# Optimization experiments

Measured on AMD Instinct MI355X. Metric: run time of the kernel, lower is better.

The kernel has to match this reference:

```python
import jax, jax.numpy as jnp
import numpy as np

EPS = 1e-5

def _conv(x, w, b, pad):
    y = jax.lax.conv_general_dilated(x, w, window_strides=(1, 1),
                                     padding=[(pad, pad), (pad, pad)],
                                     dimension_numbers=('NCHW', 'OIHW', 'NCHW'))
    return y + b[None, :, None, None]

def _bn_train(x, gamma, beta):
    # BatchNorm2d in training mode: batch statistics over (N,H,W), biased var
    mean = jnp.mean(x, axis=(0, 2, 3), keepdims=True)
    var = jnp.mean(jnp.square(x - mean), axis=(0, 2, 3), keepdims=True)
    xhat = (x - mean) * jax.lax.rsqrt(var + EPS)
    return xhat * gamma[None, :, None, None] + beta[None, :, None, None]

def _maxpool2(x):
    # CustomMaxPool2d(kernel=2) -> stride=2, no padding applied to data
    return jax.lax.reduce_window(x, -jnp.inf, jax.lax.max,
                                 (1, 1, 2, 2), (1, 1, 2, 2), 'VALID')

def setup_inputs() -> dict:
    key = jax.random.key(0)
    ks = jax.random.split(key, 12)
    B = 64
    d = jax.random.normal(ks[0], (B, 3, 224, 224), dtype=jnp.float32)
    def w_init(k, shape, fan_in):
        bound = 1.0 / np.sqrt(fan_in)
        return jax.random.uniform(k, shape, jnp.float32, -bound, bound)
    conv1_w = w_init(ks[1], (16, 3, 2, 2), 3 * 2 * 2)
    conv1_b = w_init(ks[2], (16,), 3 * 2 * 2)
    conv2_w = w_init(ks[3], (32, 16, 3, 3), 16 * 9)
    conv2_b = w_init(ks[4], (32,), 16 * 9)
    conv3_w = w_init(ks[5], (64, 32, 3, 3), 32 * 9)
    conv3_b = w_init(ks[6], (64,), 32 * 9)
    fc1_w = w_init(ks[7], (256, 64 * 28 * 28), 64 * 28 * 28)
    fc1_b = w_init(ks[8], (256,), 64 * 28 * 28)
    fc2_w = w_init(ks[9], (5, 256), 256)
    fc2_b = w_init(ks[10], (5,), 256)
    return dict(d=d,
                conv1_w=conv1_w, conv1_b=conv1_b,
                bn1_g=jnp.ones((16,), jnp.float32), bn1_b=jnp.zeros((16,), jnp.float32),
                conv2_w=conv2_w, conv2_b=conv2_b,
                bn2_g=jnp.ones((32,), jnp.float32), bn2_b=jnp.zeros((32,), jnp.float32),
                conv3_w=conv3_w, conv3_b=conv3_b,
                bn3_g=jnp.ones((64,), jnp.float32), bn3_b=jnp.zeros((64,), jnp.float32),
                fc1_w=fc1_w, fc1_b=fc1_b, fc2_w=fc2_w, fc2_b=fc2_b)

def reference(d, conv1_w, conv1_b, bn1_g, bn1_b,
              conv2_w, conv2_b, bn2_g, bn2_b,
              conv3_w, conv3_b, bn3_g, bn3_b,
              fc1_w, fc1_b, fc2_w, fc2_b):
    x = _maxpool2(jax.nn.relu(_bn_train(_conv(d, conv1_w, conv1_b, 1), bn1_g, bn1_b)))   # [B,16,112,112]
    x = _maxpool2(jax.nn.relu(_bn_train(_conv(x, conv2_w, conv2_b, 1), bn2_g, bn2_b)))   # [B,32,56,56]
    x = _maxpool2(jax.nn.relu(_bn_train(_conv(x, conv3_w, conv3_b, 1), bn3_g, bn3_b)))   # [B,64,28,28]
    x = x.reshape(x.shape[0], -1)                                                        # [B,50176]
    x = jax.nn.relu(x @ fc1_w.T + fc1_b)
    return x @ fc2_w.T + fc2_b                                                           # [B,5]
```

## Files before the change

### kernel.cpp

```cpp
#include <hip/hip_runtime.h>
#include <cstdint>
#include <cstddef>


typedef __attribute__((ext_vector_type(8))) short sh8_t;
typedef __attribute__((ext_vector_type(4))) float f4_t;
typedef unsigned short u16;
typedef unsigned int u32;

#define WS_X1   ((size_t)0)
#define WS_MX1  ((size_t)6422528)
#define WS_MN1  ((size_t)12845056)
#define WS_X2   ((size_t)19267584)
#define WS_MX2  ((size_t)22478848)
#define WS_MN2  ((size_t)25690112)
#define WS_X3T  ((size_t)28901376)
#define WS_MX3  ((size_t)30507008)
#define WS_MN3  ((size_t)32112640)
#define WS_WT1  ((size_t)33718272)
#define WS_WT2  ((size_t)33718784)
#define WS_WT3  ((size_t)33721856)
#define WS_P1   ((size_t)33731072)
#define WS_P2   ((size_t)35574272)
#define WS_P3   ((size_t)36377088)
#define WS_PD   ((size_t)36835840)
#define WS_ST   ((size_t)36839936)
#define WS_FCP  ((size_t)36840160)
#define WS_H1   ((size_t)37757664)

static __device__ __forceinline__ float4 ldg4(const float* p) {
  return *reinterpret_cast<const float4*>(p);
}
static __device__ __forceinline__ float bf2f(u16 u) {
  union { u32 i; float f; } c; c.i = ((u32)u) << 16; return c.f;
}
static __device__ __forceinline__ u16 f2bf(float f) {
  union { float f; u32 i; } c; c.f = f;
  const u32 x = c.i;
  return (u16)((x + 0x7fffu + ((x >> 16) & 1u)) >> 16);
}

__global__ __launch_bounds__(256)
void k_prep_w(const float* __restrict__ w1, const float* __restrict__ w2,
              const float* __restrict__ w3, u16* __restrict__ wt1,
              u16* __restrict__ wt2, u16* __restrict__ wt3) {
  const int t = blockIdx.x * 256 + threadIdx.x;
  if (t < 1024) {
    const int half = t >> 9;
    const int u = t & 511;
    const int co = u >> 5, k = u & 31;
    const int g = k >> 3, j = k & 7;
    const int kh = g >> 1, kw = g & 1;
    const int ci = (j < 4) ? j : j - 4;
    bool active = (j != 3) && (j != 7);
    if (half == 1) active = active && (j < 4);
    float val = 0.f;
    if (active) {
      const float w = w1[((co * 3 + ci) * 2 + kh) * 2 + kw];
      const u16 h = f2bf(w);
      val = (half == 0) ? bf2f(h) : (w - bf2f(h));
    }
    wt1[t] = f2bf(val);
  } else if (t < 7168) {
    const int u = t - 1024;
    const int ci = u & 15, kwp = (u >> 4) & 3, kh = (u >> 6) % 3, co = u / 192;
    float v = 0.f;
    if (kwp < 3) v = w2[((co * 16 + ci) * 3 + kh) * 3 + kwp];
    wt2[u] = f2bf(v);
  } else {
    const int u = t - 7168;
    const int ci = u & 31, kw = (u >> 5) % 3, kh = (u / 96) % 3, co = u / 288;
    wt3[u] = f2bf(w3[((co * 32 + ci) * 3 + kh) * 3 + kw]);
  }
}

__global__ __launch_bounds__(256)
void k_conv1(const float* __restrict__ d, const u16* __restrict__ wt1,
             const float* __restrict__ b1, u16* __restrict__ mx1,
             u16* __restrict__ mn1, float* __restrict__ part) {
  const int bx = blockIdx.x, by = blockIdx.y, n = blockIdx.z;
  const int ow0 = bx * 16, oh0 = by * 16;
  const int t = threadIdx.x, lane = t & 63, wv = t >> 6;
  const int g = lane >> 4, li = lane & 15;
  __shared__ __align__(16) u16 tile[18 * 18 * 8];
  for (int idx = t; idx < 324; idx += 256) {
    const int rr = idx / 18, cc = idx - rr * 18;
    const int ih = oh0 - 1 + rr, iw = ow0 - 1 + cc;
    float v[3] = {0.f, 0.f, 0.f};
    if ((unsigned)ih < 224u && (unsigned)iw < 224u) {
      #pragma unroll
      for (int ci = 0; ci < 3; ++ci)
        v[ci] = d[((size_t)(n * 3 + ci) * 224 + ih) * 224 + iw];
    }
    u16 rec[8];
    #pragma unroll
    for (int ci = 0; ci < 3; ++ci) {
      const u16 h = f2bf(v[ci]);
      rec[ci] = h;
      rec[4 + ci] = f2bf(v[ci] - bf2f(h));
    }
    rec[3] = 0; rec[7] = 0;
    u32 pk0 = (u32)rec[0] | ((u32)rec[1] << 16);
    u32 pk1 = (u32)rec[2] | ((u32)rec[3] << 16);
    u32 pk2 = (u32)rec[4] | ((u32)rec[5] << 16);
    u32 pk3 = (u32)rec[6] | ((u32)rec[7] << 16);
    *reinterpret_cast<int4*>(&tile[idx * 8]) = make_int4(pk0, pk1, pk2, pk3);
  }
  const sh8_t A1 = *reinterpret_cast<const sh8_t*>(wt1 + li * 32 + g * 8);
  const sh8_t A2 = *reinterpret_cast<const sh8_t*>(wt1 + 512 + li * 32 + g * 8);
  __syncthreads();
  const int kh = g >> 1, kw = g & 1;
  f4_t acc[4];
  #pragma unroll
  for (int r = 0; r < 4; ++r) acc[r] = (f4_t)0.f;
  #pragma unroll
  for (int r = 0; r < 4; ++r) {
    const int rr = wv * 4 + r + kh;
    const sh8_t B = *reinterpret_cast<const sh8_t*>(&tile[(rr * 18 + li + kw) * 8]);
    acc[r] = __builtin_amdgcn_mfma_f32_16x16x32_bf16(A1, B, acc[r], 0, 0, 0);
    acc[r] = __builtin_amdgcn_mfma_f32_16x16x32_bf16(A2, B, acc[r], 0, 0, 0);
  }
  const f4_t bias = *reinterpret_cast<const f4_t*>(b1 + 4 * g);
  f4_t y[4];
  #pragma unroll
  for (int r = 0; r < 4; ++r) y[r] = acc[r] + bias;
  const int ow = ow0 + li;
  {
    f4_t ssum = (f4_t)0.f, ssq = (f4_t)0.f;
    #pragma unroll
    for (int r = 0; r < 4; ++r) {
      const int oh = oh0 + wv * 4 + r;
      if (oh <= 224 && ow <= 224) { ssum += y[r]; ssq += y[r] * y[r]; }
    }
    #pragma unroll
    for (int m = 1; m < 16; m <<= 1)
      #pragma unroll
      for (int j = 0; j < 4; ++j) {
        ssum[j] += __shfl_xor(ssum[j], m);
        ssq[j]  += __shfl_xor(ssq[j], m);
      }
    if (li == 0) {
      const int slot = ((n * 15 + by) * 15 + bx) * 4 + wv;
      #pragma unroll
      for (int j = 0; j < 4; ++j) {
        part[(size_t)((4 * g + j) * 2 + 0) * 57600 + slot] = ssum[j];
        part[(size_t)((4 * g + j) * 2 + 1) * 57600 + slot] = ssq[j];
      }
    }
  }
  if (bx < 14 && by < 14) {
    #pragma unroll
    for (int rp = 0; rp < 2; ++rp) {
      f4_t vmax, vmin;
      #pragma unroll
      for (int j = 0; j < 4; ++j) {
        vmax[j] = fmaxf(y[2 * rp][j], y[2 * rp + 1][j]);
        vmin[j] = fminf(y[2 * rp][j], y[2 * rp + 1][j]);
      }
      f4_t omx, omn;
      #pragma unroll
      for (int j = 0; j < 4; ++j) {
        omx[j] = __shfl_xor(vmax[j], 1);
        omn[j] = __shfl_xor(vmin[j], 1);
      }
      if ((li & 1) == 0) {
        const int po = 8 * by + 2 * wv + rp, qo = 8 * bx + (li >> 1);
        const size_t off = ((size_t)((n * 112 + po) * 112 + qo)) * 16 + 4 * g;
        uint2 pmx, pmn;
        pmx.x = (u32)f2bf(fmaxf(vmax[0], omx[0])) | ((u32)f2bf(fmaxf(vmax[1], omx[1])) << 16);
        pmx.y = (u32)f2bf(fmaxf(vmax[2], omx[2])) | ((u32)f2bf(fmaxf(vmax[3], omx[3])) << 16);
        pmn.x = (u32)f2bf(fminf(vmin[0], omn[0])) | ((u32)f2bf(fminf(vmin[1], omn[1])) << 16);
        pmn.y = (u32)f2bf(fminf(vmin[2], omn[2])) | ((u32)f2bf(fminf(vmin[3], omn[3])) << 16);
        *reinterpret_cast<uint2*>(mx1 + off) = pmx;
        *reinterpret_cast<uint2*>(mn1 + off) = pmn;
      }
    }
  }
}

__global__ __launch_bounds__(256)
void k_fin1(const float* __restrict__ part, int P, int chunk, int S,
            double* __restrict__ p2) {
  const int c = blockIdx.x, s = blockIdx.y;
  const int start = s * chunk;
  const int end = min(P, start + chunk);
  __shared__ double rs[256], rq[256];
  double accs[2];
  #pragma unroll
  for (int mom = 0; mom < 2; ++mom) {
    const float* base = part + (size_t)(c * 2 + mom) * P;
    double a0 = 0.0, a1 = 0.0, a2 = 0.0, a3 = 0.0;
    int i = start + threadIdx.x * 4;
    for (; i + 3 < end; i += 1024) {
      const float4 v = ldg4(base + i);
      a0 += v.x; a1 += v.y; a2 += v.z; a3 += v.w;
    }
    for (int j = i; j < end && j < i + 4; ++j) a0 += base[j];
    accs[mom] = (a0 + a1) + (a2 + a3);
  }
  rs[threadIdx.x] = accs[0]; rq[threadIdx.x] = accs[1];
  __syncthreads();
  for (int off = 128; off > 0; off >>= 1) {
    if (threadIdx.x < off) {
      rs[threadIdx.x] += rs[threadIdx.x + off];
      rq[threadIdx.x] += rq[threadIdx.x + off];
    }
    __syncthreads();
  }
  if (threadIdx.x == 0) {
    p2[(size_t)(c * 2 + 0) * S + s] = rs[0];
    p2[(size_t)(c * 2 + 1) * S + s] = rq[0];
  }
}

__global__ __launch_bounds__(64)
void k_fin2(const double* __restrict__ p2, int S, double count,
            const float* __restrict__ g, const float* __restrict__ bta,
            float* __restrict__ scale, float* __restrict__ shift) {
  const int c = blockIdx.x, t = threadIdx.x;
  double s = 0.0, sq = 0.0;
  if (t < S) {
    s  = p2[(size_t)(c * 2 + 0) * S + t];
    sq = p2[(size_t)(c * 2 + 1) * S + t];
  }
  #pragma unroll
  for (int m = 1; m < 64; m <<= 1) {
    s  += __shfl_xor(s, m);
    sq += __shfl_xor(sq, m);
  }
  if (t == 0) {
    const double mean = s / count;
    const double var  = sq / count - mean * mean;
    const double rstd = 1.0 / sqrt(var + 1e-5);
    const double sc = (double)g[c] * rstd;
    scale[c] = (float)sc;
    shift[c] = (float)((double)bta[c] - mean * sc);
  }
}

template<int CH, int P>
__global__ __launch_bounds__(256)
void k_bnrelu(const u16* __restrict__ mx, const u16* __restrict__ mn,
              const float* __restrict__ scale, const float* __restrict__ shift,
              u16* __restrict__ xout) {
  constexpr int G = CH / 8;
  const int idx = blockIdx.x * 256 + threadIdx.x;
  const int cg = idx & (G - 1);
  int rest = idx / G;
  const int qo = rest % P; rest /= P;
  const int po = rest % P;
  const int n = rest / P;
  const size_t base = ((size_t)((n * P + po) * P + qo)) * CH + cg * 8;
  const int4 vmx = *reinterpret_cast<const int4*>(mx + base);
  const int4 vmn = *reinterpret_cast<const int4*>(mn + base);
  const u32* am = reinterpret_cast<const u32*>(&vmx);
  const u32* an = reinterpret_cast<const u32*>(&vmn);
  u16 o[8];
  #pragma unroll
  for (int j = 0; j < 8; ++j) {
    const int c = cg * 8 + j;
    const float sc = scale[c], sh = shift[c];
    const u32 src = (sc >= 0.f) ? am[j >> 1] : an[j >> 1];
    const u16 raw = (u16)(src >> ((j & 1) * 16));
    o[j] = f2bf(fmaxf(fmaf(bf2f(raw), sc, sh), 0.f));
  }
  u32 pk[4];
  #pragma unroll
  for (int k = 0; k < 4; ++k) pk[k] = (u32)o[2 * k] | ((u32)o[2 * k + 1] << 16);
  *reinterpret_cast<int4*>(xout + base) = make_int4(pk[0], pk[1], pk[2], pk[3]);
}

__global__ __launch_bounds__(256)
void k_conv2(const u16* __restrict__ x1, const u16* __restrict__ wt2,
             const float* __restrict__ b2, u16* __restrict__ mx2,
             u16* __restrict__ mn2, float* __restrict__ part) {
  const int ow0 = blockIdx.x * 16, oh0 = blockIdx.y * 16, n = blockIdx.z;
  const int t = threadIdx.x, lane = t & 63, wv = t >> 6;
  const int g = lane >> 4, li = lane & 15;
  __shared__ __align__(16) unsigned char tile[18 * 640];
  for (int idx = t; idx < 720; idx += 256) {
    const int rr = idx / 40, rem = idx - rr * 40, p = rem >> 1, c = rem & 1;
    const int ih = oh0 - 1 + rr, iw = ow0 - 1 + p;
    int4 v = make_int4(0, 0, 0, 0);
    if ((unsigned)ih < 112u && (unsigned)iw < 112u)
      v = *reinterpret_cast<const int4*>(x1 + ((size_t)((n * 112 + ih) * 112 + iw) * 16 + c * 8));
    *reinterpret_cast<int4*>(tile + ((rr * 640 + p * 32 + c * 16) ^ (((p >> 2) & 1) << 4))) = v;
  }
  sh8_t W[2][3][2];
  #pragma unroll
  for (int cot = 0; cot < 2; ++cot)
    #pragma unroll
    for (int kh = 0; kh < 3; ++kh)
      #pragma unroll
      for (int m = 0; m < 2; ++m)
        W[cot][kh][m] = *reinterpret_cast<const sh8_t*>(
            wt2 + ((cot * 16 + li) * 192 + kh * 64 + m * 32 + g * 8));
  f4_t acc[4][2];
  #pragma unroll
  for (int r = 0; r < 4; ++r) { acc[r][0] = (f4_t)0.f; acc[r][1] = (f4_t)0.f; }
  __syncthreads();
  const int rowb = 4 * wv;
  #pragma unroll
  for (int ihr = 0; ihr < 6; ++ihr) {
    const int row = rowb + ihr;
    #pragma unroll
    for (int m = 0; m < 2; ++m) {
      const int p = li + 2 * m + (g >> 1);
      const sh8_t B = *reinterpret_cast<const sh8_t*>(
          tile + ((row * 640 + p * 32 + (g & 1) * 16) ^ (((p >> 2) & 1) << 4)));
      #pragma unroll
      for (int kh = 0; kh < 3; ++kh) {
        const int r = ihr - kh;
        if (r >= 0 && r < 4) {
          acc[r][0] = __builtin_amdgcn_mfma_f32_16x16x32_bf16(W[0][kh][m], B, acc[r][0], 0, 0, 0);
          acc[r][1] = __builtin_amdgcn_mfma_f32_16x16x32_bf16(W[1][kh][m], B, acc[r][1], 0, 0, 0);
        }
      }
    }
  }
  f4_t bias[2], ssum[2], ssq[2];
  bias[0] = *reinterpret_cast<const f4_t*>(b2 + 4 * g);
  bias[1] = *reinterpret_cast<const f4_t*>(b2 + 16 + 4 * g);
  ssum[0] = (f4_t)0.f; ssum[1] = (f4_t)0.f; ssq[0] = (f4_t)0.f; ssq[1] = (f4_t)0.f;
  #pragma unroll
  for (int r = 0; r < 4; ++r)
    #pragma unroll
    for (int cot = 0; cot < 2; ++cot) {
      acc[r][cot] += bias[cot];
      ssum[cot] += acc[r][cot];
      ssq[cot] += acc[r][cot] * acc[r][cot];
    }
  #pragma unroll
  for (int msk = 1; msk < 16; msk <<= 1)
    #pragma unroll
    for (int cot = 0; cot < 2; ++cot)
      #pragma unroll
      for (int j = 0; j < 4; ++j) {
        ssum[cot][j] += __shfl_xor(ssum[cot][j], msk);
        ssq[cot][j]  += __shfl_xor(ssq[cot][j], msk);
      }
  if (li == 0) {
    const int slot = (((n * 7 + (int)blockIdx.y) * 7 + (int)blockIdx.x)) * 4 + wv;
    #pragma unroll
    for (int cot = 0; cot < 2; ++cot)
      #pragma unroll
      for (int j = 0; j < 4; ++j) {
        const int co = cot * 16 + 4 * g + j;
        part[(size_t)(co * 2 + 0) * 12544 + slot] = ssum[cot][j];
        part[(size_t)(co * 2 + 1) * 12544 + slot] = ssq[cot][j];
      }
  }
  const int pob = 8 * (int)blockIdx.y + 2 * wv;
  const int qo = 8 * (int)blockIdx.x + (li >> 1);
  #pragma unroll
  for (int rp = 0; rp < 2; ++rp)
    #pragma unroll
    for (int cot = 0; cot < 2; ++cot) {
      f4_t vmax, vmin;
      #pragma unroll
      for (int j = 0; j < 4; ++j) {
        vmax[j] = fmaxf(acc[2 * rp][cot][j], acc[2 * rp + 1][cot][j]);
        vmin[j] = fminf(acc[2 * rp][cot][j], acc[2 * rp + 1][cot][j]);
      }
      f4_t omx, omn;
      #pragma unroll
      for (int j = 0; j < 4; ++j) {
        omx[j] = __shfl_xor(vmax[j], 1);
        omn[j] = __shfl_xor(vmin[j], 1);
      }
      if ((li & 1) == 0) {
        const size_t off = ((size_t)((n * 56 + pob + rp) * 56 + qo)) * 32 + cot * 16 + 4 * g;
        uint2 pmx, pmn;
        pmx.x = (u32)f2bf(fmaxf(vmax[0], omx[0])) | ((u32)f2bf(fmaxf(vmax[1], omx[1])) << 16);
        pmx.y = (u32)f2bf(fmaxf(vmax[2], omx[2])) | ((u32)f2bf(fmaxf(vmax[3], omx[3])) << 16);
        pmn.x = (u32)f2bf(fminf(vmin[0], omn[0])) | ((u32)f2bf(fminf(vmin[1], omn[1])) << 16);
        pmn.y = (u32)f2bf(fminf(vmin[2], omn[2])) | ((u32)f2bf(fminf(vmin[3], omn[3])) << 16);
        *reinterpret_cast<uint2*>(mx2 + off) = pmx;
        *reinterpret_cast<uint2*>(mn2 + off) = pmn;
      }
    }
}

__global__ __launch_bounds__(256)
void k_conv3(const u16* __restrict__ x2, const u16* __restrict__ wt3,
             const float* __restrict__ b3, u16* __restrict__ mx3,
             u16* __restrict__ mn3, float* __restrict__ part) {
  const int ow0 = blockIdx.x * 16, oh0 = blockIdx.y * 8, n = blockIdx.z;
  const int t = threadIdx.x, lane = t & 63, wv = t >> 6;
  const int rh = wv & 1, ch = wv >> 1;
  const int g = lane >> 4, li = lane & 15;
  __shared__ __align__(16) unsigned char tile[10 * 1152];
  for (int idx = t; idx < 720; idx += 256) {
    const int rr = idx / 72, rem = idx - rr * 72, p = rem >> 2, c = rem & 3;
    const int ih = oh0 - 1 + rr, iw = ow0 - 1 + p;
    int4 v = make_int4(0, 0, 0, 0);
    if ((unsigned)ih < 56u && (unsigned)iw < 56u)
      v = *reinterpret_cast<const int4*>(x2 + ((size_t)((n * 56 + ih) * 56 + iw) * 32 + c * 8));
    *reinterpret_cast<int4*>(tile + ((rr * 1152 + p * 64 + c * 16) ^ (((p >> 1) & 3) << 4))) = v;
  }
  sh8_t W[2][3][3];
  #pragma unroll
  for (int c2 = 0; c2 < 2; ++c2)
    #pragma unroll
    for (int kh = 0; kh < 3; ++kh)
      #pragma unroll
      for (int kw = 0; kw < 3; ++kw)
        W[c2][kh][kw] = *reinterpret_cast<const sh8_t*>(
            wt3 + ((size_t)(ch * 32 + c2 * 16 + li) * 288 + (kh * 3 + kw) * 32 + g * 8));
  f4_t acc[4][2];
  #pragma unroll
  for (int r = 0; r < 4; ++r) { acc[r][0] = (f4_t)0.f; acc[r][1] = (f4_t)0.f; }
  __syncthreads();
  const int rowb = 4 * rh;
  #pragma unroll
  for (int ihr = 0; ihr < 6; ++ihr) {
    const int row = rowb + ihr;
    #pragma unroll
    for (int kw = 0; kw < 3; ++kw) {
      const int p = li + kw;
      const sh8_t B = *reinterpret_cast<const sh8_t*>(
          tile + ((row * 1152 + p * 64 + g * 16) ^ (((p >> 1) & 3) << 4)));
      #pragma unroll
      for (int kh = 0; kh < 3; ++kh) {
        const int r = ihr - kh;
        if (r >= 0 && r < 4) {
          acc[r][0] = __builtin_amdgcn_mfma_f32_16x16x32_bf16(W[0][kh][kw], B, acc[r][0], 0, 0, 0);
          acc[r][1] = __builtin_amdgcn_mfma_f32_16x16x32_bf16(W[1][kh][kw], B, acc[r][1], 0, 0, 0);
        }
      }
    }
  }
  const int ow = ow0 + li;
  const bool valid = ow < 56;
  f4_t bias[2], ssum[2], ssq[2];
  bias[0] = *reinterpret_cast<const f4_t*>(b3 + ch * 32 + 4 * g);
  bias[1] = *reinterpret_cast<const f4_t*>(b3 + ch * 32 + 16 + 4 * g);
  ssum[0] = (f4_t)0.f; ssum[1] = (f4_t)0.f; ssq[0] = (f4_t)0.f; ssq[1] = (f4_t)0.f;
  #pragma unroll
  for (int r = 0; r < 4; ++r)
    #pragma unroll
    for (int c2 = 0; c2 < 2; ++c2) {
      acc[r][c2] += bias[c2];
      if (valid) {
        ssum[c2] += acc[r][c2];
        ssq[c2] += acc[r][c2] * acc[r][c2];
      }
    }
  #pragma unroll
  for (int msk = 1; msk < 16; msk <<= 1)
    #pragma unroll
    for (int c2 = 0; c2 < 2; ++c2)
      #pragma unroll
      for (int j = 0; j < 4; ++j) {
        ssum[c2][j] += __shfl_xor(ssum[c2][j], msk);
        ssq[c2][j]  += __shfl_xor(ssq[c2][j], msk);
      }
  if (li == 0) {
    const int slot = (((n * 7 + (int)blockIdx.y) * 4 + (int)blockIdx.x)) * 2 + rh;
    #pragma unroll
    for (int c2 = 0; c2 < 2; ++c2)
      #pragma unroll
      for (int j = 0; j < 4; ++j) {
        const int co = ch * 32 + c2 * 16 + 4 * g + j;
        part[(size_t)(co * 2 + 0) * 3584 + slot] = ssum[c2][j];
        part[(size_t)(co * 2 + 1) * 3584 + slot] = ssq[c2][j];
      }
  }
  const int pob = 4 * (int)blockIdx.y + 2 * rh;
  const int qo = 8 * (int)blockIdx.x + (li >> 1);
  #pragma unroll
  for (int rp = 0; rp < 2; ++rp)
    #pragma unroll
    for (int c2 = 0; c2 < 2; ++c2) {
      f4_t vmax, vmin;
      #pragma unroll
      for (int j = 0; j < 4; ++j) {
        vmax[j] = fmaxf(acc[2 * rp][c2][j], acc[2 * rp + 1][c2][j]);
        vmin[j] = fminf(acc[2 * rp][c2][j], acc[2 * rp + 1][c2][j]);
      }
      f4_t omx, omn;
      #pragma unroll
      for (int j = 0; j < 4; ++j) {
        omx[j] = __shfl_xor(vmax[j], 1);
        omn[j] = __shfl_xor(vmin[j], 1);
      }
      if (((li & 1) == 0) && (ow + 1 < 56)) {
        const size_t off = ((size_t)((n * 28 + pob + rp) * 28 + qo)) * 64 + ch * 32 + c2 * 16 + 4 * g;
        uint2 pmx, pmn;
        pmx.x = (u32)f2bf(fmaxf(vmax[0], omx[0])) | ((u32)f2bf(fmaxf(vmax[1], omx[1])) << 16);
        pmx.y = (u32)f2bf(fmaxf(vmax[2], omx[2])) | ((u32)f2bf(fmaxf(vmax[3], omx[3])) << 16);
        pmn.x = (u32)f2bf(fminf(vmin[0], omn[0])) | ((u32)f2bf(fminf(vmin[1], omn[1])) << 16);
        pmn.y = (u32)f2bf(fminf(vmin[2], omn[2])) | ((u32)f2bf(fminf(vmin[3], omn[3])) << 16);
        *reinterpret_cast<uint2*>(mx3 + off) = pmx;
        *reinterpret_cast<uint2*>(mn3 + off) = pmn;
      }
    }
}

__global__ __launch_bounds__(256)
void k_bnrelu3t(const u16* __restrict__ mx3, const u16* __restrict__ mn3,
                const float* __restrict__ scale, const float* __restrict__ shift,
                u16* __restrict__ x3t) {
  const int n = blockIdx.y;
  const int c = threadIdx.x & 63, pq = threadIdx.x >> 6;
  const int po = blockIdx.x * 4 + pq;
  const float sc = scale[c], sh = shift[c];
  const bool useMax = (sc >= 0.f);
  const size_t row0 = ((size_t)(n * 28 + po)) * 28 * 64 + c;
  #pragma unroll
  for (int q4 = 0; q4 < 7; ++q4) {
    u16 pk[4];
    #pragma unroll
    for (int i = 0; i < 4; ++i) {
      const int qo = q4 * 4 + i;
      const size_t b = row0 + (size_t)qo * 64;
      const u16 raw = useMax ? mx3[b] : mn3[b];
      pk[i] = f2bf(fmaxf(fmaf(bf2f(raw), sc, sh), 0.f));
    }
    uint2 w;
    w.x = (u32)pk[0] | ((u32)pk[1] << 16);
    w.y = (u32)pk[2] | ((u32)pk[3] << 16);
    *reinterpret_cast<uint2*>(x3t + (((size_t)(n * 64 + c) * 28 + po) * 28 + q4 * 4)) = w;
  }
}

__global__ __launch_bounds__(256)
void k_fc1(const u16* __restrict__ x3t, const float* __restrict__ w,
           float* __restrict__ partial) {
  const int kc = blockIdx.x, nt = blockIdx.y;
  const int t = threadIdx.x, lane = t & 63, wv = t >> 6;
  const int g = lane >> 4, li = lane & 15;
  const int n0 = nt * 64 + wv * 16;
  const float* wrow = w + (size_t)(n0 + li) * 50176 + kc * 896;
  const u16* xbase = x3t + kc * 896;
  f4_t acc[4];
  #pragma unroll
  for (int mf = 0; mf < 4; ++mf) acc[mf] = (f4_t)0.f;
  #pragma unroll 4
  for (int ks = 0; ks < 28; ++ks) {
    const int kb = ks * 32 + g * 8;
    const float4 wa = ldg4(wrow + kb);
    const float4 wb = ldg4(wrow + kb + 4);
    float wf[8] = {wa.x, wa.y, wa.z, wa.w, wb.x, wb.y, wb.z, wb.w};
    sh8_t hi, lo;
    #pragma unroll
    for (int j = 0; j < 8; ++j) {
      const u16 h = f2bf(wf[j]);
      hi[j] = (short)h;
      lo[j] = (short)f2bf(wf[j] - bf2f(h));
    }
    #pragma unroll
    for (int mf = 0; mf < 4; ++mf) {
      const sh8_t B = *reinterpret_cast<const sh8_t*>(
          xbase + (size_t)(mf * 16 + li) * 50176 + kb);
      acc[mf] = __builtin_amdgcn_mfma_f32_16x16x32_bf16(hi, B, acc[mf], 0, 0, 0);
      acc[mf] = __builtin_amdgcn_mfma_f32_16x16x32_bf16(lo, B, acc[mf], 0, 0, 0);
    }
  }
  float* pb = partial + (size_t)kc * 16384;
  #pragma unroll
  for (int mf = 0; mf < 4; ++mf)
    #pragma unroll
    for (int j = 0; j < 4; ++j)
      pb[(size_t)(n0 + 4 * g + j) * 64 + mf * 16 + li] = acc[mf][j];
}

__global__ __launch_bounds__(256)
void k_fc1_reduce(const float* __restrict__ partial, const float* __restrict__ b1f,
                  float* __restrict__ h1) {
  const int idx = blockIdx.x * 256 + threadIdx.x;
  const int nn = idx >> 6, m = idx & 63;
  float a[8];
  #pragma unroll
  for (int u = 0; u < 8; ++u) a[u] = 0.f;
  #pragma unroll
  for (int k = 0; k < 56; k += 8)
    #pragma unroll
    for (int u = 0; u < 8; ++u)
      a[u] += partial[(size_t)(k + u) * 16384 + idx];
  const float s = b1f[nn] + (((a[0] + a[1]) + (a[2] + a[3])) +
                             ((a[4] + a[5]) + (a[6] + a[7])));
  h1[(size_t)m * 256 + nn] = fmaxf(s, 0.f);
}

__global__ __launch_bounds__(320)
void k_fc2(const float* __restrict__ h1, const float* __restrict__ w2f,
           const float* __restrict__ b2f, float* __restrict__ out) {
  const int t = threadIdx.x;
  const int m = t / 5, o = t - m * 5;
  const float* hr = h1 + (size_t)m * 256;
  const float* wr = w2f + (size_t)o * 256;
  float a0 = 0.f, a1 = 0.f, a2 = 0.f, a3 = 0.f;
  #pragma unroll
  for (int j = 0; j < 256; j += 16) {
    const float4 h0 = ldg4(hr + j),      w0 = ldg4(wr + j);
    const float4 h1v = ldg4(hr + j + 4),  w1v = ldg4(wr + j + 4);
    const float4 h2 = ldg4(hr + j + 8),  w2 = ldg4(wr + j + 8);
    const float4 h3 = ldg4(hr + j + 12), w3 = ldg4(wr + j + 12);
    a0 = fmaf(h0.x, w0.x, fmaf(h0.y, w0.y, fmaf(h0.z, w0.z, fmaf(h0.w, w0.w, a0))));
    a1 = fmaf(h1v.x, w1v.x, fmaf(h1v.y, w1v.y, fmaf(h1v.z, w1v.z, fmaf(h1v.w, w1v.w, a1))));
    a2 = fmaf(h2.x, w2.x, fmaf(h2.y, w2.y, fmaf(h2.z, w2.z, fmaf(h2.w, w2.w, a2))));
    a3 = fmaf(h3.x, w3.x, fmaf(h3.y, w3.y, fmaf(h3.z, w3.z, fmaf(h3.w, w3.w, a3))));
  }
  out[m * 5 + o] = b2f[o] + ((a0 + a1) + (a2 + a3));
}

extern "C" void kernel_launch(void* const* d_in, const int* in_sizes, int n_in,
                              void* d_out, int out_size, void* d_ws, size_t ws_size,
                              hipStream_t stream) {
  (void)in_sizes; (void)n_in; (void)out_size; (void)ws_size;
  const float* d   = (const float*)d_in[0];
  const float* w1  = (const float*)d_in[1];
  const float* b1  = (const float*)d_in[2];
  const float* g1  = (const float*)d_in[3];
  const float* be1 = (const float*)d_in[4];
  const float* w2  = (const float*)d_in[5];
  const float* b2  = (const float*)d_in[6];
  const float* g2  = (const float*)d_in[7];
  const float* be2 = (const float*)d_in[8];
  const float* w3  = (const float*)d_in[9];
  const float* b3  = (const float*)d_in[10];
  const float* g3  = (const float*)d_in[11];
  const float* be3 = (const float*)d_in[12];
  const float* fw1 = (const float*)d_in[13];
  const float* fb1 = (const float*)d_in[14];
  const float* fw2 = (const float*)d_in[15];
  const float* fb2 = (const float*)d_in[16];
  float* out = (float*)d_out;
  float* ws  = (float*)d_ws;

  u16* x1   = (u16*)(ws + WS_X1);
  u16* mx1  = (u16*)(ws + WS_MX1);
  u16* mn1  = (u16*)(ws + WS_MN1);
  u16* x2   = (u16*)(ws + WS_X2);
  u16* mx2  = (u16*)(ws + WS_MX2);
  u16* mn2  = (u16*)(ws + WS_MN2);
  u16* x3t  = (u16*)(ws + WS_X3T);
  u16* mx3  = (u16*)(ws + WS_MX3);
  u16* mn3  = (u16*)(ws + WS_MN3);
  u16* wt1  = (u16*)(ws + WS_WT1);
  u16* wt2  = (u16*)(ws + WS_WT2);
  u16* wt3  = (u16*)(ws + WS_WT3);
  float* p1 = ws + WS_P1;
  float* p2 = ws + WS_P2;
  float* p3 = ws + WS_P3;
  double* pd = (double*)(ws + WS_PD);
  float* st = ws + WS_ST;
  float* fcp = ws + WS_FCP;
  float* h1 = ws + WS_H1;

  k_prep_w<<<100, 256, 0, stream>>>(w1, w2, w3, wt1, wt2, wt3);
  k_conv1<<<dim3(15, 15, 64), 256, 0, stream>>>(d, wt1, b1, mx1, mn1, p1);
  k_fin1<<<dim3(16, 64), 256, 0, stream>>>(p1, 57600, 900, 64, pd);
  k_fin2<<<16, 64, 0, stream>>>(pd, 64, 3240000.0, g1, be1, st + 0, st + 16);
  k_bnrelu<16, 112><<<6272, 256, 0, stream>>>(mx1, mn1, st + 0, st + 16, x1);
  k_conv2<<<dim3(7, 7, 64), 256, 0, stream>>>(x1, wt2, b2, mx2, mn2, p2);
  k_fin1<<<dim3(32, 16), 256, 0, stream>>>(p2, 12544, 784, 16, pd);
  k_fin2<<<32, 64, 0, stream>>>(pd, 16, 802816.0, g2, be2, st + 32, st + 64);
  k_bnrelu<32, 56><<<3136, 256, 0, stream>>>(mx2, mn2, st + 32, st + 64, x2);
  k_conv3<<<dim3(4, 7, 64), 256, 0, stream>>>(x2, wt3, b3, mx3, mn3, p3);
  k_fin1<<<dim3(64, 8), 256, 0, stream>>>(p3, 3584, 448, 8, pd);
  k_fin2<<<64, 64, 0, stream>>>(pd, 8, 200704.0, g3, be3, st + 96, st + 160);
  k_bnrelu3t<<<dim3(7, 64), 256, 0, stream>>>(mx3, mn3, st + 96, st + 160, x3t);
  k_fc1<<<dim3(56, 4), 256, 0, stream>>>(x3t, fw1, fcp);
  k_fc1_reduce<<<64, 256, 0, stream>>>(fcp, fb1, h1);
  k_fc2<<<1, 320, 0, stream>>>(h1, fw2, fb2, out);
}
```

Measured before the change: 187.3 us.

## Precompute bf16 hi/lo packed input records in separate kernel for conv1

Adds a pre-pass kernel that converts the fp32 NCHW input into per-pixel packed bf16 hi/lo channel records (16 bytes each), using vectorized float4 loads. conv1 then drops its shared-memory staging, the split conversion and the barrier, and loads MFMA B operands straight from global memory with bounds masking. The record buffer reuses workspace meant for later layers. The aim is to replace scattered scalar input loads and per-tile conversion with coalesced 16-byte loads. The cost is an extra launch and a larger intermediate that must be written and then read back.

```diff
diff --git a/kernel.cpp b/kernel.cpp
--- a/kernel.cpp
+++ b/kernel.cpp
@@ -17,6 +17,7 @@
 #define WS_X3T  ((size_t)28901376)
 #define WS_MX3  ((size_t)30507008)
 #define WS_MN3  ((size_t)32112640)
+#define WS_REC  WS_X2
 #define WS_WT1  ((size_t)33718272)
 #define WS_WT2  ((size_t)33718784)
 #define WS_WT3  ((size_t)33721856)
@@ -75,48 +76,55 @@
 }
 
 __global__ __launch_bounds__(256)
-void k_conv1(const float* __restrict__ d, const u16* __restrict__ wt1,
+void k_prep_rec(const float* __restrict__ d, u16* __restrict__ rec) {
+  const int t = blockIdx.x * 256 + threadIdx.x;
+  const int px4 = t * 4;
+  const int n = px4 / 50176;
+  const int remn = px4 - n * 50176;
+  const float4 v0 = ldg4(d + (size_t)(n * 3 + 0) * 50176 + remn);
+  const float4 v1 = ldg4(d + (size_t)(n * 3 + 1) * 50176 + remn);
+  const float4 v2 = ldg4(d + (size_t)(n * 3 + 2) * 50176 + remn);
+  const float* c0 = reinterpret_cast<const float*>(&v0);
+  const float* c1 = reinterpret_cast<const float*>(&v1);
+  const float* c2 = reinterpret_cast<const float*>(&v2);
+  #pragma unroll
+  for (int i = 0; i < 4; ++i) {
+    const float a = c0[i], b = c1[i], c = c2[i];
+    const u16 h0 = f2bf(a), h1 = f2bf(b), h2 = f2bf(c);
+    const u16 l0 = f2bf(a - bf2f(h0));
+    const u16 l1 = f2bf(b - bf2f(h1));
+    const u16 l2 = f2bf(c - bf2f(h2));
+    int4 r;
+    r.x = (u32)h0 | ((u32)h1 << 16);
+    r.y = (u32)h2;
+    r.z = (u32)l0 | ((u32)l1 << 16);
+    r.w = (u32)l2;
+    *reinterpret_cast<int4*>(rec + (size_t)(px4 + i) * 8) = r;
+  }
+}
+
+__global__ __launch_bounds__(256)
+void k_conv1(const u16* __restrict__ rec, const u16* __restrict__ wt1,
              const float* __restrict__ b1, u16* __restrict__ mx1,
              u16* __restrict__ mn1, float* __restrict__ part) {
   const int bx = blockIdx.x, by = blockIdx.y, n = blockIdx.z;
   const int ow0 = bx * 16, oh0 = by * 16;
   const int t = threadIdx.x, lane = t & 63, wv = t >> 6;
   const int g = lane >> 4, li = lane & 15;
-  __shared__ __align__(16) u16 tile[18 * 18 * 8];
-  for (int idx = t; idx < 324; idx += 256) {
-    const int rr = idx / 18, cc = idx - rr * 18;
-    const int ih = oh0 - 1 + rr, iw = ow0 - 1 + cc;
-    float v[3] = {0.f, 0.f, 0.f};
-    if ((unsigned)ih < 224u && (unsigned)iw < 224u) {
-      #pragma unroll
-      for (int ci = 0; ci < 3; ++ci)
-        v[ci] = d[((size_t)(n * 3 + ci) * 224 + ih) * 224 + iw];
-    }
-    u16 rec[8];
-    #pragma unroll
-    for (int ci = 0; ci < 3; ++ci) {
-      const u16 h = f2bf(v[ci]);
-      rec[ci] = h;
-      rec[4 + ci] = f2bf(v[ci] - bf2f(h));
-    }
-    rec[3] = 0; rec[7] = 0;
-    u32 pk0 = (u32)rec[0] | ((u32)rec[1] << 16);
-    u32 pk1 = (u32)rec[2] | ((u32)rec[3] << 16);
-    u32 pk2 = (u32)rec[4] | ((u32)rec[5] << 16);
-    u32 pk3 = (u32)rec[6] | ((u32)rec[7] << 16);
-    *reinterpret_cast<int4*>(&tile[idx * 8]) = make_int4(pk0, pk1, pk2, pk3);
-  }
+  const int kh = g >> 1, kw = g & 1;
   const sh8_t A1 = *reinterpret_cast<const sh8_t*>(wt1 + li * 32 + g * 8);
   const sh8_t A2 = *reinterpret_cast<const sh8_t*>(wt1 + 512 + li * 32 + g * 8);
-  __syncthreads();
-  const int kh = g >> 1, kw = g & 1;
+  const int iw = ow0 + li + kw - 1;
+  const bool iwv = (unsigned)iw < 224u;
   f4_t acc[4];
   #pragma unroll
   for (int r = 0; r < 4; ++r) acc[r] = (f4_t)0.f;
   #pragma unroll
   for (int r = 0; r < 4; ++r) {
-    const int rr = wv * 4 + r + kh;
-    const sh8_t B = *reinterpret_cast<const sh8_t*>(&tile[(rr * 18 + li + kw) * 8]);
+    const int ih = oh0 + wv * 4 + r + kh - 1;
+    sh8_t B = (sh8_t)(short)0;
+    if (iwv && (unsigned)ih < 224u)
+      B = *reinterpret_cast<const sh8_t*>(rec + ((size_t)(n * 224 + ih) * 224 + iw) * 8);
     acc[r] = __builtin_amdgcn_mfma_f32_16x16x32_bf16(A1, B, acc[r], 0, 0, 0);
     acc[r] = __builtin_amdgcn_mfma_f32_16x16x32_bf16(A2, B, acc[r], 0, 0, 0);
   }
@@ -632,6 +640,7 @@
   u16* x1   = (u16*)(ws + WS_X1);
   u16* mx1  = (u16*)(ws + WS_MX1);
   u16* mn1  = (u16*)(ws + WS_MN1);
+  u16* rec  = (u16*)(ws + WS_REC);
   u16* x2   = (u16*)(ws + WS_X2);
   u16* mx2  = (u16*)(ws + WS_MX2);
   u16* mn2  = (u16*)(ws + WS_MN2);
@@ -650,7 +659,8 @@
   float* h1 = ws + WS_H1;
 
   k_prep_w<<<100, 256, 0, stream>>>(w1, w2, w3, wt1, wt2, wt3);
-  k_conv1<<<dim3(15, 15, 64), 256, 0, stream>>>(d, wt1, b1, mx1, mn1, p1);
+  k_prep_rec<<<3136, 256, 0, stream>>>(d, rec);
+  k_conv1<<<dim3(15, 15, 64), 256, 0, stream>>>(rec, wt1, b1, mx1, mn1, p1);
   k_fin1<<<dim3(16, 64), 256, 0, stream>>>(p1, 57600, 900, 64, pd);
   k_fin2<<<16, 64, 0, stream>>>(pd, 64, 3240000.0, g1, be1, st + 0, st + 16);
   k_bnrelu<16, 112><<<6272, 256, 0, stream>>>(mx1, mn1, st + 0, st + 16, x1);
```

Result: slower. 203.4 us (+8.6%).

## Select max/min pool by gamma sign in conv epilogues; read conv1 input directly

Applied to the files above, without the earlier changes.

Because BN scale = gamma*rstd and rstd > 0, the sign of gamma decides whether max or min pooling commutes with the affine BN. Each conv epilogue therefore writes one pooled tensor chosen per channel by gamma's sign, instead of both max and min tensors. This halves the pooled intermediate writes and the reads in the bnrelu kernels. Conv1 also drops its shared-memory tile staging and builds the MFMA B operands straight from global loads, removing a __syncthreads but making more uncoalesced, redundant global reads.

```diff
diff --git a/kernel.cpp b/kernel.cpp
--- a/kernel.cpp
+++ b/kernel.cpp
@@ -9,24 +9,21 @@
 typedef unsigned int u32;
 
 #define WS_X1   ((size_t)0)
-#define WS_MX1  ((size_t)6422528)
-#define WS_MN1  ((size_t)12845056)
-#define WS_X2   ((size_t)19267584)
-#define WS_MX2  ((size_t)22478848)
-#define WS_MN2  ((size_t)25690112)
-#define WS_X3T  ((size_t)28901376)
-#define WS_MX3  ((size_t)30507008)
-#define WS_MN3  ((size_t)32112640)
-#define WS_WT1  ((size_t)33718272)
-#define WS_WT2  ((size_t)33718784)
-#define WS_WT3  ((size_t)33721856)
-#define WS_P1   ((size_t)33731072)
-#define WS_P2   ((size_t)35574272)
-#define WS_P3   ((size_t)36377088)
-#define WS_PD   ((size_t)36835840)
-#define WS_ST   ((size_t)36839936)
-#define WS_FCP  ((size_t)36840160)
-#define WS_H1   ((size_t)37757664)
+#define WS_SEL1 ((size_t)6422528)
+#define WS_X2   ((size_t)12845056)
+#define WS_SEL2 ((size_t)16056320)
+#define WS_X3T  ((size_t)19267584)
+#define WS_SEL3 ((size_t)20873216)
+#define WS_WT1  ((size_t)22478848)
+#define WS_WT2  ((size_t)22479360)
+#define WS_WT3  ((size_t)22482432)
+#define WS_P1   ((size_t)22491648)
+#define WS_P2   ((size_t)24334848)
+#define WS_P3   ((size_t)25137664)
+#define WS_PD   ((size_t)25596416)
+#define WS_ST   ((size_t)25600512)
+#define WS_FCP  ((size_t)25600736)
+#define WS_H1   ((size_t)26518240)
 
 static __device__ __forceinline__ float4 ldg4(const float* p) {
   return *reinterpret_cast<const float4*>(p);
@@ -76,51 +73,43 @@
 
 __global__ __launch_bounds__(256)
 void k_conv1(const float* __restrict__ d, const u16* __restrict__ wt1,
-             const float* __restrict__ b1, u16* __restrict__ mx1,
-             u16* __restrict__ mn1, float* __restrict__ part) {
+             const float* __restrict__ b1, const float* __restrict__ g1,
+             u16* __restrict__ sel1, float* __restrict__ part) {
   const int bx = blockIdx.x, by = blockIdx.y, n = blockIdx.z;
   const int ow0 = bx * 16, oh0 = by * 16;
   const int t = threadIdx.x, lane = t & 63, wv = t >> 6;
   const int g = lane >> 4, li = lane & 15;
-  __shared__ __align__(16) u16 tile[18 * 18 * 8];
-  for (int idx = t; idx < 324; idx += 256) {
-    const int rr = idx / 18, cc = idx - rr * 18;
-    const int ih = oh0 - 1 + rr, iw = ow0 - 1 + cc;
-    float v[3] = {0.f, 0.f, 0.f};
-    if ((unsigned)ih < 224u && (unsigned)iw < 224u) {
-      #pragma unroll
-      for (int ci = 0; ci < 3; ++ci)
-        v[ci] = d[((size_t)(n * 3 + ci) * 224 + ih) * 224 + iw];
-    }
-    u16 rec[8];
-    #pragma unroll
-    for (int ci = 0; ci < 3; ++ci) {
-      const u16 h = f2bf(v[ci]);
-      rec[ci] = h;
-      rec[4 + ci] = f2bf(v[ci] - bf2f(h));
-    }
-    rec[3] = 0; rec[7] = 0;
-    u32 pk0 = (u32)rec[0] | ((u32)rec[1] << 16);
-    u32 pk1 = (u32)rec[2] | ((u32)rec[3] << 16);
-    u32 pk2 = (u32)rec[4] | ((u32)rec[5] << 16);
-    u32 pk3 = (u32)rec[6] | ((u32)rec[7] << 16);
-    *reinterpret_cast<int4*>(&tile[idx * 8]) = make_int4(pk0, pk1, pk2, pk3);
-  }
+  const int kh = g >> 1, kw = g & 1;
   const sh8_t A1 = *reinterpret_cast<const sh8_t*>(wt1 + li * 32 + g * 8);
   const sh8_t A2 = *reinterpret_cast<const sh8_t*>(wt1 + 512 + li * 32 + g * 8);
-  __syncthreads();
-  const int kh = g >> 1, kw = g & 1;
+  const int iw = ow0 + li + kw - 1;
+  const bool iwv = (unsigned)iw < 224u;
+  const float* dbase = d + (size_t)n * 3 * 50176 + iw;
   f4_t acc[4];
   #pragma unroll
   for (int r = 0; r < 4; ++r) acc[r] = (f4_t)0.f;
   #pragma unroll
   for (int r = 0; r < 4; ++r) {
-    const int rr = wv * 4 + r + kh;
-    const sh8_t B = *reinterpret_cast<const sh8_t*>(&tile[(rr * 18 + li + kw) * 8]);
-    acc[r] = __builtin_amdgcn_mfma_f32_16x16x32_bf16(A1, B, acc[r], 0, 0, 0);
-    acc[r] = __builtin_amdgcn_mfma_f32_16x16x32_bf16(A2, B, acc[r], 0, 0, 0);
+    const int ih = oh0 + wv * 4 + r + kh - 1;
+    float v0 = 0.f, v1 = 0.f, v2 = 0.f;
+    if (iwv && (unsigned)ih < 224u) {
+      const float* p = dbase + (size_t)ih * 224;
+      v0 = p[0]; v1 = p[50176]; v2 = p[100352];
+    }
+    const u16 h0 = f2bf(v0), h1 = f2bf(v1), h2 = f2bf(v2);
+    const u16 l0 = f2bf(v0 - bf2f(h0));
+    const u16 l1 = f2bf(v1 - bf2f(h1));
+    const u16 l2 = f2bf(v2 - bf2f(h2));
+    union { sh8_t v; u32 w[4]; } B;
+    B.w[0] = (u32)h0 | ((u32)h1 << 16);
+    B.w[1] = (u32)h2;
+    B.w[2] = (u32)l0 | ((u32)l1 << 16);
+    B.w[3] = (u32)l2;
+    acc[r] = __builtin_amdgcn_mfma_f32_16x16x32_bf16(A1, B.v, acc[r], 0, 0, 0);
+    acc[r] = __builtin_amdgcn_mfma_f32_16x16x32_bf16(A2, B.v, acc[r], 0, 0, 0);
   }
   const f4_t bias = *reinterpret_cast<const f4_t*>(b1 + 4 * g);
+  const f4_t gam  = *reinterpret_cast<const f4_t*>(g1 + 4 * g);
   f4_t y[4];
   #pragma unroll
   for (int r = 0; r < 4; ++r) y[r] = acc[r] + bias;
@@ -151,28 +140,26 @@
   if (bx < 14 && by < 14) {
     #pragma unroll
     for (int rp = 0; rp < 2; ++rp) {
-      f4_t vmax, vmin;
-      #pragma unroll
-      for (int j = 0; j < 4; ++j) {
-        vmax[j] = fmaxf(y[2 * rp][j], y[2 * rp + 1][j]);
-        vmin[j] = fminf(y[2 * rp][j], y[2 * rp + 1][j]);
-      }
-      f4_t omx, omn;
-      #pragma unroll
-      for (int j = 0; j < 4; ++j) {
-        omx[j] = __shfl_xor(vmax[j], 1);
-        omn[j] = __shfl_xor(vmin[j], 1);
-      }
+      f4_t v;
+      #pragma unroll
+      for (int j = 0; j < 4; ++j) {
+        const float a = y[2 * rp][j], b = y[2 * rp + 1][j];
+        v[j] = (gam[j] >= 0.f) ? fmaxf(a, b) : fminf(a, b);
+      }
+      f4_t o;
+      #pragma unroll
+      for (int j = 0; j < 4; ++j) o[j] = __shfl_xor(v[j], 1);
       if ((li & 1) == 0) {
+        u16 pk[4];
+        #pragma unroll
+        for (int j = 0; j < 4; ++j)
+          pk[j] = f2bf((gam[j] >= 0.f) ? fmaxf(v[j], o[j]) : fminf(v[j], o[j]));
         const int po = 8 * by + 2 * wv + rp, qo = 8 * bx + (li >> 1);
         const size_t off = ((size_t)((n * 112 + po) * 112 + qo)) * 16 + 4 * g;
-        uint2 pmx, pmn;
-        pmx.x = (u32)f2bf(fmaxf(vmax[0], omx[0])) | ((u32)f2bf(fmaxf(vmax[1], omx[1])) << 16);
-        pmx.y = (u32)f2bf(fmaxf(vmax[2], omx[2])) | ((u32)f2bf(fmaxf(vmax[3], omx[3])) << 16);
-        pmn.x = (u32)f2bf(fminf(vmin[0], omn[0])) | ((u32)f2bf(fminf(vmin[1], omn[1])) << 16);
-        pmn.y = (u32)f2bf(fminf(vmin[2], omn[2])) | ((u32)f2bf(fminf(vmin[3], omn[3])) << 16);
-        *reinterpret_cast<uint2*>(mx1 + off) = pmx;
-        *reinterpret_cast<uint2*>(mn1 + off) = pmn;
+        uint2 w;
+        w.x = (u32)pk[0] | ((u32)pk[1] << 16);
+        w.y = (u32)pk[2] | ((u32)pk[3] << 16);
+        *reinterpret_cast<uint2*>(sel1 + off) = w;
       }
     }
   }
@@ -240,9 +227,8 @@
 
 template<int CH, int P>
 __global__ __launch_bounds__(256)
-void k_bnrelu(const u16* __restrict__ mx, const u16* __restrict__ mn,
-              const float* __restrict__ scale, const float* __restrict__ shift,
-              u16* __restrict__ xout) {
+void k_bnrelu(const u16* __restrict__ sel, const float* __restrict__ scale,
+              const float* __restrict__ shift, u16* __restrict__ xout) {
   constexpr int G = CH / 8;
   const int idx = blockIdx.x * 256 + threadIdx.x;
   const int cg = idx & (G - 1);
@@ -251,17 +237,14 @@
   const int po = rest % P;
   const int n = rest / P;
   const size_t base = ((size_t)((n * P + po) * P + qo)) * CH + cg * 8;
-  const int4 vmx = *reinterpret_cast<const int4*>(mx + base);
-  const int4 vmn = *reinterpret_cast<const int4*>(mn + base);
-  const u32* am = reinterpret_cast<const u32*>(&vmx);
-  const u32* an = reinterpret_cast<const u32*>(&vmn);
+  const int4 vs = *reinterpret_cast<const int4*>(sel + base);
+  const u32* a = reinterpret_cast<const u32*>(&vs);
   u16 o[8];
   #pragma unroll
   for (int j = 0; j < 8; ++j) {
     const int c = cg * 8 + j;
     const float sc = scale[c], sh = shift[c];
-    const u32 src = (sc >= 0.f) ? am[j >> 1] : an[j >> 1];
-    const u16 raw = (u16)(src >> ((j & 1) * 16));
+    const u16 raw = (u16)(a[j >> 1] >> ((j & 1) * 16));
     o[j] = f2bf(fmaxf(fmaf(bf2f(raw), sc, sh), 0.f));
   }
   u32 pk[4];
@@ -272,8 +255,8 @@
 
 __global__ __launch_bounds__(256)
 void k_conv2(const u16* __restrict__ x1, const u16* __restrict__ wt2,
-             const float* __restrict__ b2, u16* __restrict__ mx2,
-             u16* __restrict__ mn2, float* __restrict__ part) {
+             const float* __restrict__ b2, const float* __restrict__ g2,
+             u16* __restrict__ sel2, float* __restrict__ part) {
   const int ow0 = blockIdx.x * 16, oh0 = blockIdx.y * 16, n = blockIdx.z;
   const int t = threadIdx.x, lane = t & 63, wv = t >> 6;
   const int g = lane >> 4, li = lane & 15;
@@ -318,9 +301,11 @@
       }
     }
   }
-  f4_t bias[2], ssum[2], ssq[2];
+  f4_t bias[2], gam[2], ssum[2], ssq[2];
   bias[0] = *reinterpret_cast<const f4_t*>(b2 + 4 * g);
   bias[1] = *reinterpret_cast<const f4_t*>(b2 + 16 + 4 * g);
+  gam[0]  = *reinterpret_cast<const f4_t*>(g2 + 4 * g);
+  gam[1]  = *reinterpret_cast<const f4_t*>(g2 + 16 + 4 * g);
   ssum[0] = (f4_t)0.f; ssum[1] = (f4_t)0.f; ssq[0] = (f4_t)0.f; ssq[1] = (f4_t)0.f;
   #pragma unroll
   for (int r = 0; r < 4; ++r)
@@ -356,35 +341,33 @@
   for (int rp = 0; rp < 2; ++rp)
     #pragma unroll
     for (int cot = 0; cot < 2; ++cot) {
-      f4_t vmax, vmin;
-      #pragma unroll
-      for (int j = 0; j < 4; ++j) {
-        vmax[j] = fmaxf(acc[2 * rp][cot][j], acc[2 * rp + 1][cot][j]);
-        vmin[j] = fminf(acc[2 * rp][cot][j], acc[2 * rp + 1][cot][j]);
-      }
-      f4_t omx, omn;
-      #pragma unroll
-      for (int j = 0; j < 4; ++j) {
-        omx[j] = __shfl_xor(vmax[j], 1);
-        omn[j] = __shfl_xor(vmin[j], 1);
-      }
+      f4_t v;
+      #pragma unroll
+      for (int j = 0; j < 4; ++j) {
+        const float a = acc[2 * rp][cot][j], b = acc[2 * rp + 1][cot][j];
+        v[j] = (gam[cot][j] >= 0.f) ? fmaxf(a, b) : fminf(a, b);
+      }
+      f4_t o;
+      #pragma unroll
+      for (int j = 0; j < 4; ++j) o[j] = __shfl_xor(v[j], 1);
       if ((li & 1) == 0) {
+        u16 pk[4];
+        #pragma unroll
+        for (int j = 0; j < 4; ++j)
+          pk[j] = f2bf((gam[cot][j] >= 0.f) ? fmaxf(v[j], o[j]) : fminf(v[j], o[j]));
         const size_t off = ((size_t)((n * 56 + pob + rp) * 56 + qo)) * 32 + cot * 16 + 4 * g;
-        uint2 pmx, pmn;
-        pmx.x = (u32)f2bf(fmaxf(vmax[0], omx[0])) | ((u32)f2bf(fmaxf(vmax[1], omx[1])) << 16);
-        pmx.y = (u32)f2bf(fmaxf(vmax[2], omx[2])) | ((u32)f2bf(fmaxf(vmax[3], omx[3])) << 16);
-        pmn.x = (u32)f2bf(fminf(vmin[0], omn[0])) | ((u32)f2bf(fminf(vmin[1], omn[1])) << 16);
-        pmn.y = (u32)f2bf(fminf(vmin[2], omn[2])) | ((u32)f2bf(fminf(vmin[3], omn[3])) << 16);
-        *reinterpret_cast<uint2*>(mx2 + off) = pmx;
-        *reinterpret_cast<uint2*>(mn2 + off) = pmn;
+        uint2 w;
+        w.x = (u32)pk[0] | ((u32)pk[1] << 16);
+        w.y = (u32)pk[2] | ((u32)pk[3] << 16);
+        *reinterpret_cast<uint2*>(sel2 + off) = w;
       }
     }
 }
 
 __global__ __launch_bounds__(256)
 void k_conv3(const u16* __restrict__ x2, const u16* __restrict__ wt3,
-             const float* __restrict__ b3, u16* __restrict__ mx3,
-             u16* __restrict__ mn3, float* __restrict__ part) {
+             const float* __restrict__ b3, const float* __restrict__ g3,
+             u16* __restrict__ sel3, float* __restrict__ part) {
   const int ow0 = blockIdx.x * 16, oh0 = blockIdx.y * 8, n = blockIdx.z;
   const int t = threadIdx.x, lane = t & 63, wv = t >> 6;
   const int rh = wv & 1, ch = wv >> 1;
@@ -432,9 +415,11 @@
   }
   const int ow = ow0 + li;
   const bool valid = ow < 56;
-  f4_t bias[2], ssum[2], ssq[2];
+  f4_t bias[2], gam[2], ssum[2], ssq[2];
   bias[0] = *reinterpret_cast<const f4_t*>(b3 + ch * 32 + 4 * g);
   bias[1] = *reinterpret_cast<const f4_t*>(b3 + ch * 32 + 16 + 4 * g);
+  gam[0]  = *reinterpret_cast<const f4_t*>(g3 + ch * 32 + 4 * g);
+  gam[1]  = *reinterpret_cast<const f4_t*>(g3 + ch * 32 + 16 + 4 * g);
   ssum[0] = (f4_t)0.f; ssum[1] = (f4_t)0.f; ssq[0] = (f4_t)0.f; ssq[1] = (f4_t)0.f;
   #pragma unroll
   for (int r = 0; r < 4; ++r)
@@ -472,40 +457,36 @@
   for (int rp = 0; rp < 2; ++rp)
     #pragma unroll
     for (int c2 = 0; c2 < 2; ++c2) {
-      f4_t vmax, vmin;
-      #pragma unroll
-      for (int j = 0; j < 4; ++j) {
-        vmax[j] = fmaxf(acc[2 * rp][c2][j], acc[2 * rp + 1][c2][j]);
-        vmin[j] = fminf(acc[2 * rp][c2][j], acc[2 * rp + 1][c2][j]);
-      }
-      f4_t omx, omn;
-      #pragma unroll
-      for (int j = 0; j < 4; ++j) {
-        omx[j] = __shfl_xor(vmax[j], 1);
-        omn[j] = __shfl_xor(vmin[j], 1);
-      }
+      f4_t v;
+      #pragma unroll
+      for (int j = 0; j < 4; ++j) {
+        const float a = acc[2 * rp][c2][j], b = acc[2 * rp + 1][c2][j];
+        v[j] = (gam[c2][j] >= 0.f) ? fmaxf(a, b) : fminf(a, b);
+      }
+      f4_t o;
+      #pragma unroll
+      for (int j = 0; j < 4; ++j) o[j] = __shfl_xor(v[j], 1);
       if (((li & 1) == 0) && (ow + 1 < 56)) {
+        u16 pk[4];
+        #pragma unroll
+        for (int j = 0; j < 4; ++j)
+          pk[j] = f2bf((gam[c2][j] >= 0.f) ? fmaxf(v[j], o[j]) : fminf(v[j], o[j]));
         const size_t off = ((size_t)((n * 28 + pob + rp) * 28 + qo)) * 64 + ch * 32 + c2 * 16 + 4 * g;
-        uint2 pmx, pmn;
-        pmx.x = (u32)f2bf(fmaxf(vmax[0], omx[0])) | ((u32)f2bf(fmaxf(vmax[1], omx[1])) << 16);
-        pmx.y = (u32)f2bf(fmaxf(vmax[2], omx[2])) | ((u32)f2bf(fmaxf(vmax[3], omx[3])) << 16);
-        pmn.x = (u32)f2bf(fminf(vmin[0], omn[0])) | ((u32)f2bf(fminf(vmin[1], omn[1])) << 16);
-        pmn.y = (u32)f2bf(fminf(vmin[2], omn[2])) | ((u32)f2bf(fminf(vmin[3], omn[3])) << 16);
-        *reinterpret_cast<uint2*>(mx3 + off) = pmx;
-        *reinterpret_cast<uint2*>(mn3 + off) = pmn;
-      }
-    }
-}
-
-__global__ __launch_bounds__(256)
-void k_bnrelu3t(const u16* __restrict__ mx3, const u16* __restrict__ mn3,
-                const float* __restrict__ scale, const float* __restrict__ shift,
-                u16* __restrict__ x3t) {
+        uint2 w;
+        w.x = (u32)pk[0] | ((u32)pk[1] << 16);
+        w.y = (u32)pk[2] | ((u32)pk[3] << 16);
+        *reinterpret_cast<uint2*>(sel3 + off) = w;
+      }
+    }
+}
+
+__global__ __launch_bounds__(256)
+void k_bnrelu3t(const u16* __restrict__ sel3, const float* __restrict__ scale,
+                const float* __restrict__ shift, u16* __restrict__ x3t) {
   const int n = blockIdx.y;
   const int c = threadIdx.x & 63, pq = threadIdx.x >> 6;
   const int po = blockIdx.x * 4 + pq;
   const float sc = scale[c], sh = shift[c];
-  const bool useMax = (sc >= 0.f);
   const size_t row0 = ((size_t)(n * 28 + po)) * 28 * 64 + c;
   #pragma unroll
   for (int q4 = 0; q4 < 7; ++q4) {
@@ -513,8 +494,7 @@
     #pragma unroll
     for (int i = 0; i < 4; ++i) {
       const int qo = q4 * 4 + i;
-      const size_t b = row0 + (size_t)qo * 64;
-      const u16 raw = useMax ? mx3[b] : mn3[b];
+      const u16 raw = sel3[row0 + (size_t)qo * 64];
       pk[i] = f2bf(fmaxf(fmaf(bf2f(raw), sc, sh), 0.f));
     }
     uint2 w;
@@ -630,14 +610,11 @@
   float* ws  = (float*)d_ws;
 
   u16* x1   = (u16*)(ws + WS_X1);
-  u16* mx1  = (u16*)(ws + WS_MX1);
-  u16* mn1  = (u16*)(ws + WS_MN1);
+  u16* sel1 = (u16*)(ws + WS_SEL1);
   u16* x2   = (u16*)(ws + WS_X2);
-  u16* mx2  = (u16*)(ws + WS_MX2);
-  u16* mn2  = (u16*)(ws + WS_MN2);
+  u16* sel2 = (u16*)(ws + WS_SEL2);
   u16* x3t  = (u16*)(ws + WS_X3T);
-  u16* mx3  = (u16*)(ws + WS_MX3);
-  u16* mn3  = (u16*)(ws + WS_MN3);
+  u16* sel3 = (u16*)(ws + WS_SEL3);
   u16* wt1  = (u16*)(ws + WS_WT1);
   u16* wt2  = (u16*)(ws + WS_WT2);
   u16* wt3  = (u16*)(ws + WS_WT3);
@@ -650,18 +627,18 @@
   float* h1 = ws + WS_H1;
 
   k_prep_w<<<100, 256, 0, stream>>>(w1, w2, w3, wt1, wt2, wt3);
-  k_conv1<<<dim3(15, 15, 64), 256, 0, stream>>>(d, wt1, b1, mx1, mn1, p1);
+  k_conv1<<<dim3(15, 15, 64), 256, 0, stream>>>(d, wt1, b1, g1, sel1, p1);
   k_fin1<<<dim3(16, 64), 256, 0, stream>>>(p1, 57600, 900, 64, pd);
   k_fin2<<<16, 64, 0, stream>>>(pd, 64, 3240000.0, g1, be1, st + 0, st + 16);
-  k_bnrelu<16, 112><<<6272, 256, 0, stream>>>(mx1, mn1, st + 0, st + 16, x1);
-  k_conv2<<<dim3(7, 7, 64), 256, 0, stream>>>(x1, wt2, b2, mx2, mn2, p2);
+  k_bnrelu<16, 112><<<6272, 256, 0, stream>>>(sel1, st + 0, st + 16, x1);
+  k_conv2<<<dim3(7, 7, 64), 256, 0, stream>>>(x1, wt2, b2, g2, sel2, p2);
   k_fin1<<<dim3(32, 16), 256, 0, stream>>>(p2, 12544, 784, 16, pd);
   k_fin2<<<32, 64, 0, stream>>>(pd, 16, 802816.0, g2, be2, st + 32, st + 64);
-  k_bnrelu<32, 56><<<3136, 256, 0, stream>>>(mx2, mn2, st + 32, st + 64, x2);
-  k_conv3<<<dim3(4, 7, 64), 256, 0, stream>>>(x2, wt3, b3, mx3, mn3, p3);
+  k_bnrelu<32, 56><<<3136, 256, 0, stream>>>(sel2, st + 32, st + 64, x2);
+  k_conv3<<<dim3(4, 7, 64), 256, 0, stream>>>(x2, wt3, b3, g3, sel3, p3);
   k_fin1<<<dim3(64, 8), 256, 0, stream>>>(p3, 3584, 448, 8, pd);
   k_fin2<<<64, 64, 0, stream>>>(pd, 8, 200704.0, g3, be3, st + 96, st + 160);
-  k_bnrelu3t<<<dim3(7, 64), 256, 0, stream>>>(mx3, mn3, st + 96, st + 160, x3t);
+  k_bnrelu3t<<<dim3(7, 64), 256, 0, stream>>>(sel3, st + 96, st + 160, x3t);
   k_fc1<<<dim3(56, 4), 256, 0, stream>>>(x3t, fw1, fcp);
   k_fc1_reduce<<<64, 256, 0, stream>>>(fcp, fb1, h1);
   k_fc2<<<1, 320, 0, stream>>>(h1, fw2, fb2, out);
```

After: 181.5 us. 1.03x faster.
